# Optimization experiments

Measured on AMD Instinct MI355X. Metric: run time of the kernel, lower is better.

## Reference

```python
import jax, jax.numpy as jnp
import numpy as np

SEQ, BATCH, HIDDEN = 4096, 16, 512

def setup_inputs() -> dict:
    key = jax.random.key(0)
    kf, kx, kh = jax.random.split(key, 3)
    f = jax.random.uniform(kf, (SEQ, BATCH, HIDDEN), dtype=jnp.float32)
    x = jax.random.normal(kx, (SEQ, BATCH, HIDDEN), dtype=jnp.float32)
    hidden_init = jax.random.normal(kh, (BATCH, HIDDEN), dtype=jnp.float32)
    return {"f": f, "x": x, "hidden_init": hidden_init}

def reference(f, x, hidden_init):
    # h_t = f_t * x_t + (1 - f_t) * h_{t-1}
    # Linear recurrence h_t = a_t * h_{t-1} + b_t with a = 1-f, b = f*x.
    # Solved with an associative scan: compose (a1,b1) then (a2,b2) ->
    # (a1*a2, a2*b1 + b2). After the scan, A_t = prod(a_1..a_t) and
    # B_t = h_t assuming h_0 = 0, so h_t = B_t + A_t * h_init.
    a = 1.0 - f                      # (S, B, H)
    b = f * x                        # (S, B, H)

    def combine(c1, c2):
        a1, b1 = c1
        a2, b2 = c2
        return (a1 * a2, a2 * b1 + b2)

    A, B = jax.lax.associative_scan(combine, (a, b), axis=0)
    return B + A * hidden_init[None, :, :]
```

## Files before the change

### kernel.cpp

```cpp
#include <hip/hip_runtime.h>


#define SQ      4096
#define NC4     2048
#define NCH     8192

typedef float floatx4 __attribute__((ext_vector_type(4)));

template<int TT_>
__global__ __launch_bounds__(256, 4)
void fm_agg(const float4* __restrict__ f4, const float4* __restrict__ x4,
            float4* __restrict__ aggA, float4* __restrict__ aggB)
{
  const int tid   = threadIdx.x;
  const int chunk = blockIdx.x >> 3;
  const int col   = ((blockIdx.x & 7) << 8) + tid;
  const size_t base = (size_t)(chunk * TT_) * NC4 + col;

  float ax = 1.f, ay = 1.f, az = 1.f, aw = 1.f;
  float bx = 0.f, by = 0.f, bz = 0.f, bw = 0.f;

  for (int batch = 0; batch < TT_ / 8; ++batch) {
    float4 ff[8], xx[8];
#pragma unroll
    for (int i = 0; i < 8; ++i) {
      const size_t idx = base + (size_t)(batch * 8 + i) * NC4;
      ff[i] = f4[idx];
      xx[i] = x4[idx];
    }
#pragma unroll
    for (int i = 0; i < 8; ++i) {
      bx = fmaf(ff[i].x, xx[i].x - bx, bx);
      by = fmaf(ff[i].y, xx[i].y - by, by);
      bz = fmaf(ff[i].z, xx[i].z - bz, bz);
      bw = fmaf(ff[i].w, xx[i].w - bw, bw);
      ax = fmaf(-ff[i].x, ax, ax);
      ay = fmaf(-ff[i].y, ay, ay);
      az = fmaf(-ff[i].z, az, az);
      aw = fmaf(-ff[i].w, aw, aw);
    }
  }
  float4 A; A.x = ax; A.y = ay; A.z = az; A.w = aw;
  float4 B; B.x = bx; B.y = by; B.z = bz; B.w = bw;
  aggA[(size_t)chunk * NC4 + col] = A;
  aggB[(size_t)chunk * NC4 + col] = B;
}

template<int NCHUNK_>
__global__ __launch_bounds__(256, 4)
void fm_mid(const float* __restrict__ A, float* __restrict__ B,
            const float* __restrict__ h0)
{
  const int chain = blockIdx.x * 256 + threadIdx.x;
  float h = h0[chain];
  for (int cb = 0; cb < NCHUNK_ / 16; ++cb) {
    float a[16], b[16];
#pragma unroll
    for (int i = 0; i < 16; ++i) {
      const size_t idx = (size_t)(cb * 16 + i) * NCH + chain;
      a[i] = A[idx];
      b[i] = B[idx];
    }
#pragma unroll
    for (int i = 0; i < 16; ++i) {
      const size_t idx = (size_t)(cb * 16 + i) * NCH + chain;
      B[idx] = h;
      h = fmaf(a[i], h, b[i]);
    }
  }
}

template<int TT_>
__global__ __launch_bounds__(256, 4)
void fm_apply(const float4* __restrict__ f4, const float4* __restrict__ x4,
              const float4* __restrict__ hprev4, float4* __restrict__ out4)
{
  const int NCHUNK_ = SQ / TT_;
  const int tid   = threadIdx.x;
  const int chunk = (NCHUNK_ - 1) - (blockIdx.x >> 3);
  const int col   = ((blockIdx.x & 7) << 8) + tid;
  const size_t base = (size_t)(chunk * TT_) * NC4 + col;

  floatx4* __restrict__ outv = (floatx4*)out4;

  float4 h = hprev4[(size_t)chunk * NC4 + col];
  for (int batch = 0; batch < TT_ / 8; ++batch) {
    float4 ff[8], xx[8];
#pragma unroll
    for (int i = 0; i < 8; ++i) {
      const size_t idx = base + (size_t)(batch * 8 + i) * NC4;
      ff[i] = f4[idx];
      xx[i] = x4[idx];
    }
#pragma unroll
    for (int i = 0; i < 8; ++i) {
      h.x = fmaf(ff[i].x, xx[i].x - h.x, h.x);
      h.y = fmaf(ff[i].y, xx[i].y - h.y, h.y);
      h.z = fmaf(ff[i].z, xx[i].z - h.z, h.z);
      h.w = fmaf(ff[i].w, xx[i].w - h.w, h.w);
      floatx4 hv; hv.x = h.x; hv.y = h.y; hv.z = h.z; hv.w = h.w;
      __builtin_nontemporal_store(hv, &outv[base + (size_t)(batch * 8 + i) * NC4]);
    }
  }
}

__global__ void fm_naive(const float4* __restrict__ f4, const float4* __restrict__ x4,
                         const float4* __restrict__ h04, float4* __restrict__ out4)
{
  const int col = blockIdx.x * blockDim.x + threadIdx.x;
  if (col >= NC4) return;
  float4 h = h04[col];
  for (int t = 0; t < SQ; ++t) {
    const size_t idx = (size_t)t * NC4 + col;
    const float4 ff = f4[idx], xx = x4[idx];
    h.x = fmaf(ff.x, xx.x - h.x, h.x);
    h.y = fmaf(ff.y, xx.y - h.y, h.y);
    h.z = fmaf(ff.z, xx.z - h.z, h.z);
    h.w = fmaf(ff.w, xx.w - h.w, h.w);
    out4[idx] = h;
  }
}

extern "C" void kernel_launch(void* const* d_in, const int* in_sizes, int n_in,
                              void* d_out, int out_size, void* d_ws, size_t ws_size,
                              hipStream_t stream)
{
  const float4* f4  = (const float4*)d_in[0];
  const float4* x4  = (const float4*)d_in[1];
  const float4* h04 = (const float4*)d_in[2];
  float4* out4 = (float4*)d_out;

  const size_t AGG16 = (size_t)(SQ / 16) * NC4 * 16;
  const size_t AGG32 = (size_t)(SQ / 32) * NC4 * 16;

  if (ws_size >= 2 * AGG16) {
    float4* aggA = (float4*)d_ws;
    float4* aggB = (float4*)((char*)d_ws + AGG16);
    fm_agg<16><<<(SQ / 16) * 8, 256, 0, stream>>>(f4, x4, aggA, aggB);
    fm_mid<SQ / 16><<<NCH / 256, 256, 0, stream>>>((const float*)aggA,
                                                   (float*)aggB, (const float*)h04);
    fm_apply<16><<<(SQ / 16) * 8, 256, 0, stream>>>(f4, x4, (const float4*)aggB, out4);
  } else if (ws_size >= 2 * AGG32) {
    float4* aggA = (float4*)d_ws;
    float4* aggB = (float4*)((char*)d_ws + AGG32);
    fm_agg<32><<<(SQ / 32) * 8, 256, 0, stream>>>(f4, x4, aggA, aggB);
    fm_mid<SQ / 32><<<NCH / 256, 256, 0, stream>>>((const float*)aggA,
                                                   (float*)aggB, (const float*)h04);
    fm_apply<32><<<(SQ / 32) * 8, 256, 0, stream>>>(f4, x4, (const float4*)aggB, out4);
  } else {
    fm_naive<<<(NC4 + 255) / 256, 256, 0, stream>>>(f4, x4, h04, out4);
  }
}
```

Measured before the change: 366.7 us.

## Fuse aggregate, carry and apply phases into one cooperative kernel

Replaces the three-launch chunked scan with a single cooperative kernel that computes per-chunk aggregates, runs the sequential carry pass, and applies the recurrence, separated by grid-wide syncs. This removes two kernel launch gaps and lets each block revisit its own tiles in reverse order. The grid size comes from an occupancy query, with a fallback to the old path if cooperative launch fails. Grid syncs add barrier cost, and the serial mid phase still uses only a few blocks while the rest wait.

```diff
diff --git a/kernel.cpp b/kernel.cpp
--- a/kernel.cpp
+++ b/kernel.cpp
@@ -1,11 +1,118 @@
 #include <hip/hip_runtime.h>
+#include <hip/hip_cooperative_groups.h>
+
+namespace cg = cooperative_groups;
 
 
 #define SQ      4096
 #define NC4     2048
 #define NCH     8192
+#define TT      16
+#define NCHUNK  (SQ / TT)
+#define NTILE   (NCHUNK * 8)
 
 typedef float floatx4 __attribute__((ext_vector_type(4)));
+
+__global__ __launch_bounds__(256, 8)
+void fm_fused(const float4* __restrict__ f4, const float4* __restrict__ x4,
+              const float* __restrict__ h0,
+              float4* __restrict__ aggA, float4* __restrict__ aggB,
+              float4* __restrict__ out4)
+{
+  cg::grid_group grid = cg::this_grid();
+  const int tid = threadIdx.x;
+  const int G   = gridDim.x;
+
+  for (int tile = blockIdx.x; tile < NTILE; tile += G) {
+    const int chunk = tile >> 3;
+    const int col   = ((tile & 7) << 8) + tid;
+    const size_t base = (size_t)(chunk * TT) * NC4 + col;
+
+    float ax = 1.f, ay = 1.f, az = 1.f, aw = 1.f;
+    float bx = 0.f, by = 0.f, bz = 0.f, bw = 0.f;
+    for (int batch = 0; batch < TT / 8; ++batch) {
+      float4 ff[8], xx[8];
+#pragma unroll
+      for (int i = 0; i < 8; ++i) {
+        const size_t idx = base + (size_t)(batch * 8 + i) * NC4;
+        ff[i] = f4[idx];
+        xx[i] = x4[idx];
+      }
+#pragma unroll
+      for (int i = 0; i < 8; ++i) {
+        bx = fmaf(ff[i].x, xx[i].x - bx, bx);
+        by = fmaf(ff[i].y, xx[i].y - by, by);
+        bz = fmaf(ff[i].z, xx[i].z - bz, bz);
+        bw = fmaf(ff[i].w, xx[i].w - bw, bw);
+        ax = fmaf(-ff[i].x, ax, ax);
+        ay = fmaf(-ff[i].y, ay, ay);
+        az = fmaf(-ff[i].z, az, az);
+        aw = fmaf(-ff[i].w, aw, aw);
+      }
+    }
+    float4 A; A.x = ax; A.y = ay; A.z = az; A.w = aw;
+    float4 B; B.x = bx; B.y = by; B.z = bz; B.w = bw;
+    aggA[(size_t)chunk * NC4 + col] = A;
+    aggB[(size_t)chunk * NC4 + col] = B;
+  }
+
+  grid.sync();
+
+  {
+    const int chain = blockIdx.x * 256 + tid;
+    if (chain < NCH) {
+      const float* __restrict__ As = (const float*)aggA;
+      float*                   Bs = (float*)aggB;
+      float h = h0[chain];
+      for (int cb = 0; cb < NCHUNK / 16; ++cb) {
+        float a[16], b[16];
+#pragma unroll
+        for (int i = 0; i < 16; ++i) {
+          const size_t idx = (size_t)(cb * 16 + i) * NCH + chain;
+          a[i] = As[idx];
+          b[i] = Bs[idx];
+        }
+#pragma unroll
+        for (int i = 0; i < 16; ++i) {
+          const size_t idx = (size_t)(cb * 16 + i) * NCH + chain;
+          Bs[idx] = h;
+          h = fmaf(a[i], h, b[i]);
+        }
+      }
+    }
+  }
+
+  grid.sync();
+
+  floatx4* __restrict__ outv = (floatx4*)out4;
+  const int kmax = (NTILE - 1 - blockIdx.x) / G;
+  for (int k = kmax; k >= 0; --k) {
+    const int tile  = blockIdx.x + k * G;
+    const int chunk = tile >> 3;
+    const int col   = ((tile & 7) << 8) + tid;
+    const size_t base = (size_t)(chunk * TT) * NC4 + col;
+
+    float4 h = aggB[(size_t)chunk * NC4 + col];
+    for (int batch = 0; batch < TT / 8; ++batch) {
+      float4 ff[8], xx[8];
+#pragma unroll
+      for (int i = 0; i < 8; ++i) {
+        const size_t idx = base + (size_t)(batch * 8 + i) * NC4;
+        ff[i] = f4[idx];
+        xx[i] = x4[idx];
+      }
+#pragma unroll
+      for (int i = 0; i < 8; ++i) {
+        h.x = fmaf(ff[i].x, xx[i].x - h.x, h.x);
+        h.y = fmaf(ff[i].y, xx[i].y - h.y, h.y);
+        h.z = fmaf(ff[i].z, xx[i].z - h.z, h.z);
+        h.w = fmaf(ff[i].w, xx[i].w - h.w, h.w);
+        floatx4 hv; hv.x = h.x; hv.y = h.y; hv.z = h.z; hv.w = h.w;
+        __builtin_nontemporal_store(hv, &outv[base + (size_t)(batch * 8 + i) * NC4]);
+      }
+    }
+  }
+}
 
 template<int TT_>
 __global__ __launch_bounds__(256, 4)
@@ -19,7 +126,6 @@
 
   float ax = 1.f, ay = 1.f, az = 1.f, aw = 1.f;
   float bx = 0.f, by = 0.f, bz = 0.f, bw = 0.f;
-
   for (int batch = 0; batch < TT_ / 8; ++batch) {
     float4 ff[8], xx[8];
 #pragma unroll
@@ -82,7 +188,6 @@
   const size_t base = (size_t)(chunk * TT_) * NC4 + col;
 
   floatx4* __restrict__ outv = (floatx4*)out4;
-
   float4 h = hprev4[(size_t)chunk * NC4 + col];
   for (int batch = 0; batch < TT_ / 8; ++batch) {
     float4 ff[8], xx[8];
@@ -130,16 +235,48 @@
   const float4* h04 = (const float4*)d_in[2];
   float4* out4 = (float4*)d_out;
 
-  const size_t AGG16 = (size_t)(SQ / 16) * NC4 * 16;
+  const size_t AGG16 = (size_t)NCHUNK * NC4 * 16;
   const size_t AGG32 = (size_t)(SQ / 32) * NC4 * 16;
+
+  static int  coopGrid = -2;
+  if (coopGrid == -2) {
+    int dev = 0;
+    hipGetDevice(&dev);
+    hipDeviceProp_t prop;
+    int blocksPerCU = 0;
+    if (hipGetDeviceProperties(&prop, dev) == hipSuccess &&
+        prop.cooperativeLaunch &&
+        hipOccupancyMaxActiveBlocksPerMultiprocessor(
+            &blocksPerCU, (const void*)fm_fused, 256, 0) == hipSuccess &&
+        blocksPerCU > 0) {
+      long long g = (long long)blocksPerCU * prop.multiProcessorCount;
+      if (g > NTILE) g = NTILE;
+      coopGrid = (g >= 32) ? (int)g : 0;
+    } else {
+      coopGrid = 0;
+    }
+  }
+
+  if (ws_size >= 2 * AGG16 && coopGrid > 0) {
+    float4* aggA = (float4*)d_ws;
+    float4* aggB = (float4*)((char*)d_ws + AGG16);
+    void* args[6];
+    args[0] = (void*)&f4;  args[1] = (void*)&x4;  args[2] = (void*)&h04;
+    args[3] = (void*)&aggA; args[4] = (void*)&aggB; args[5] = (void*)&out4;
+    hipError_t e = hipLaunchCooperativeKernel((const void*)fm_fused,
+                                              dim3(coopGrid), dim3(256),
+                                              args, 0, stream);
+    if (e == hipSuccess) return;
+    coopGrid = 0;
+  }
 
   if (ws_size >= 2 * AGG16) {
     float4* aggA = (float4*)d_ws;
     float4* aggB = (float4*)((char*)d_ws + AGG16);
-    fm_agg<16><<<(SQ / 16) * 8, 256, 0, stream>>>(f4, x4, aggA, aggB);
-    fm_mid<SQ / 16><<<NCH / 256, 256, 0, stream>>>((const float*)aggA,
-                                                   (float*)aggB, (const float*)h04);
-    fm_apply<16><<<(SQ / 16) * 8, 256, 0, stream>>>(f4, x4, (const float4*)aggB, out4);
+    fm_agg<16><<<NTILE, 256, 0, stream>>>(f4, x4, aggA, aggB);
+    fm_mid<NCHUNK><<<NCH / 256, 256, 0, stream>>>((const float*)aggA,
+                                                  (float*)aggB, (const float*)h04);
+    fm_apply<16><<<NTILE, 256, 0, stream>>>(f4, x4, (const float4*)aggB, out4);
   } else if (ws_size >= 2 * AGG32) {
     float4* aggA = (float4*)d_ws;
     float4* aggB = (float4*)((char*)d_ws + AGG32);
```

Measured after the change: 623.0 us. 69.9% more time.
